# Optimization experiments

Hardware: AMD Instinct MI355X
Metric: run time of the kernel (lower is better)

## Reference

```python
import jax, jax.numpy as jnp
import numpy as np

VOCAB, HIDDEN, EMBED = 100000, 512, 256
N, L = 128, 2048


def setup_inputs() -> dict:
    key = jax.random.key(0)
    k1, k2, k3, k4 = jax.random.split(key, 4)
    X = jax.random.randint(k1, (N, L), 0, VOCAB)
    E = jax.random.normal(k2, (VOCAB, EMBED), dtype=jnp.float32) * 0.02
    # torch Linear: weight (out, in) = (4H, H+E), y = x @ W.T + b
    W_w = jax.random.normal(k3, (4 * HIDDEN, HIDDEN + EMBED), dtype=jnp.float32) * 0.02
    W_b = jax.random.normal(k4, (4 * HIDDEN,), dtype=jnp.float32) * 0.02
    return {"X": X, "E": E, "W_w": W_w, "W_b": W_b}


def reference(X, E, W_w, W_b):
    H = HIDDEN
    Xe = E[X]                      # (N, L, EMBED) embedding lookup
    Xe_t = jnp.transpose(Xe, (1, 0, 2))  # (L, N, EMBED) for scan over time
    n = X.shape[0]
    C0 = jnp.zeros((n, H), dtype=E.dtype)
    H0 = jnp.zeros((n, H), dtype=E.dtype)

    def step(carry, x_t):
        C, Hs = carry
        HcatX = jnp.concatenate([Hs, x_t], axis=1)       # (N, H+E)
        G = HcatX @ W_w.T + W_b                          # (N, 4H)
        F = jax.nn.sigmoid(G[:, :H])
        I = jax.nn.sigmoid(G[:, H:2 * H])
        O = jax.nn.sigmoid(G[:, 2 * H:3 * H])
        Ht = jnp.tanh(G[:, 3 * H:4 * H])
        C_new = F * C + I * Ht
        H_new = O * jnp.tanh(C_new)
        return (C_new, H_new), None

    (C_last, H_last), _ = jax.lax.scan(step, (C0, H0), Xe_t)
    return H_last
```

## Files before the change

kernel.cpp:

```cpp
#include <hip/hip_runtime.h>

#define NB   128
#define LSEQ 2048
#define HID  512
#define EMB  256
#define KD   768
#define NGRP  8
#define NPG   16
#define HBLK  32
#define HPB   16
#define NWG   256
#define NTHR  512
#define RING  4
#define KSL   96
#define FPAD  64
#define SENT 0xFFFFFFFFFFFFFFFFull

#define AT_RLX __ATOMIC_RELAXED
#define SCOPE  __HIP_MEMORY_SCOPE_AGENT

typedef unsigned long long ull;
typedef _Float16 f16;
typedef f16   f16x8 __attribute__((ext_vector_type(8)));
typedef float f32x4 __attribute__((ext_vector_type(4)));

__device__ __forceinline__ float sigf(float x) { return 1.0f / (1.0f + __expf(-x)); }
__device__ __forceinline__ float tanhfast(float x) { return fmaf(-2.0f, 1.0f / (1.0f + __expf(2.0f * x)), 1.0f); }

__device__ __forceinline__ void publish_flag(int* fl, int val, int is_l0) {
    __builtin_amdgcn_s_waitcnt(0);
    if (is_l0) __hip_atomic_store(fl, val, AT_RLX, SCOPE);
}

__global__ void __launch_bounds__(NTHR, 2)
lstm_pers(const int* __restrict__ X, const float* __restrict__ E,
          const float* __restrict__ Ww, const float* __restrict__ Wb,
          float* __restrict__ out, float* __restrict__ ws)
{
    const int tid  = threadIdx.x;
    const int bid  = blockIdx.x;
    const int ng   = bid & (NGRP - 1);
    const int hb   = bid >> 3;
    const int w    = tid >> 6;
    const int lane = tid & 63;
    const int quad = lane >> 4;
    const int m16  = lane & 15;
    const int ks   = w * KSL;
    const int koff = quad * 8;

    __shared__ float red[8][4][16][20];

    f16* Hbuf  = (f16*)ws;
    int* flags = (int*)((char*)ws + (size_t)NGRP * RING * HBLK * NPG * HPB * 2);

    f16x8 wf[4][3];
    #pragma unroll
    for (int g = 0; g < 4; ++g) {
        #pragma unroll
        for (int ti = 0; ti < 3; ++ti) {
            const float* wp = Ww + (size_t)(g * HID + hb * HPB + m16) * KD
                                 + (ks + ti * 32 + koff);
            f16x8 v;
            #pragma unroll
            for (int j = 0; j < 8; ++j) v[j] = (f16)wp[j];
            wf[g][ti] = v;
        }
    }
    f32x4 bias[4], cst = {0, 0, 0, 0};
    if (w == 7) {
        #pragma unroll
        for (int g = 0; g < 4; ++g)
            bias[g] = *(const f32x4*)(Wb + g * HID + hb * HPB + quad * 4);
        #pragma unroll
        for (int s = 2; s <= 3; ++s) {
            ull* z = (ull*)(Hbuf + ((size_t)(ng * RING + s) * HBLK + hb)
                            * (NPG * HPB) + lane * 4);
            __hip_atomic_store(z, SENT, AT_RLX, SCOPE);
        }
    }
    __syncthreads();

    const int* fp6 = flags + (size_t)(ng * HBLK + (lane & (HBLK - 1))) * FPAD;
    int* myflag = &flags[(ng * HBLK + hb) * FPAD];
    const int nh = (ks + 64 < HID) ? 3 : ((ks < HID) ? 1 : 0);

    for (int t = 0; t < LSEQ; ++t) {
        f16x8 bf[3];
        if (ks + 64 >= HID) {
            int xi = X[(ng * NPG + m16) * LSEQ + t];
            const float* eb = E + (size_t)xi * EMB;
            #pragma unroll
            for (int ti = 0; ti < 3; ++ti) {
                int k0 = ks + ti * 32;
                if (k0 >= HID) {
                    const float* ep = eb + (k0 - HID) + koff;
                    f32x4 e0 = *(const f32x4*)(ep);
                    f32x4 e1 = *(const f32x4*)(ep + 4);
                    f16x8 v;
                    #pragma unroll
                    for (int j = 0; j < 4; ++j) { v[j] = (f16)e0[j]; v[4 + j] = (f16)e1[j]; }
                    bf[ti] = v;
                }
            }
        }
        if (w == 6 && t == 1) {
            while (!__all(__hip_atomic_load(fp6, AT_RLX, SCOPE) >= 1))
                __builtin_amdgcn_s_sleep(1);
        }
        __syncthreads();
        if (t == 0) {
            f16x8 z;
            #pragma unroll
            for (int j = 0; j < 8; ++j) z[j] = (f16)0.0f;
            for (int ti = 0; ti < nh; ++ti) bf[ti] = z;
        } else if (nh == 3) {
            const f16* Hc = Hbuf + (size_t)(ng * RING + (t & 3)) * HBLK * (NPG * HPB);
            int ka = ks + koff, kb = ka + 32, kc = kb + 32;
            const ull* h0 = (const ull*)(Hc + (size_t)(ka >> 4) * (NPG * HPB) + m16 * HPB + (ka & 15));
            const ull* h1 = (const ull*)(Hc + (size_t)(kb >> 4) * (NPG * HPB) + m16 * HPB + (kb & 15));
            const ull* h2 = (const ull*)(Hc + (size_t)(kc >> 4) * (NPG * HPB) + m16 * HPB + (kc & 15));
            ull u0, u1, u2, u3, u4, u5;
            for (;;) {
                u0 = __hip_atomic_load(h0,     AT_RLX, SCOPE);
                u1 = __hip_atomic_load(h0 + 1, AT_RLX, SCOPE);
                u2 = __hip_atomic_load(h1,     AT_RLX, SCOPE);
                u3 = __hip_atomic_load(h1 + 1, AT_RLX, SCOPE);
                u4 = __hip_atomic_load(h2,     AT_RLX, SCOPE);
                u5 = __hip_atomic_load(h2 + 1, AT_RLX, SCOPE);
                bool ok = (u0 != SENT) & (u1 != SENT) & (u2 != SENT)
                        & (u3 != SENT) & (u4 != SENT) & (u5 != SENT);
                if (__all(ok)) break;
                __builtin_amdgcn_s_sleep(1);
            }
            union { ull u[2]; f16x8 v; } c;
            c.u[0] = u0; c.u[1] = u1; bf[0] = c.v;
            c.u[0] = u2; c.u[1] = u3; bf[1] = c.v;
            c.u[0] = u4; c.u[1] = u5; bf[2] = c.v;
        } else if (nh == 1) {
            const f16* Hc = Hbuf + (size_t)(ng * RING + (t & 3)) * HBLK * (NPG * HPB);
            int ka = ks + koff;
            const ull* h0 = (const ull*)(Hc + (size_t)(ka >> 4) * (NPG * HPB) + m16 * HPB + (ka & 15));
            ull u0, u1;
            for (;;) {
                u0 = __hip_atomic_load(h0,     AT_RLX, SCOPE);
                u1 = __hip_atomic_load(h0 + 1, AT_RLX, SCOPE);
                if (__all((u0 != SENT) & (u1 != SENT))) break;
                __builtin_amdgcn_s_sleep(1);
            }
            union { ull u[2]; f16x8 v; } c;
            c.u[0] = u0; c.u[1] = u1; bf[0] = c.v;
        }
        f32x4 acc[4] = {{0,0,0,0},{0,0,0,0},{0,0,0,0},{0,0,0,0}};
        #pragma unroll
        for (int ti = 0; ti < 3; ++ti)
            #pragma unroll
            for (int g = 0; g < 4; ++g)
                acc[g] = __builtin_amdgcn_mfma_f32_16x16x32_f16(wf[g][ti], bf[ti], acc[g], 0, 0, 0);

        #pragma unroll
        for (int g = 0; g < 4; ++g)
            *(f32x4*)&red[w][g][m16][quad * 4] = acc[g];
        __syncthreads();

        if (w == 7) {
            f32x4 G[4];
            #pragma unroll
            for (int g = 0; g < 4; ++g) {
                f32x4 s = bias[g];
                #pragma unroll
                for (int wv = 0; wv < 8; ++wv) {
                    f32x4 r = *(const f32x4*)&red[wv][g][m16][quad * 4];
                    s.x += r.x; s.y += r.y; s.z += r.z; s.w += r.w;
                }
                G[g] = s;
            }
            union { f16 h[4]; ull u; } pk;
            f32x4 ov;
            #pragma unroll
            for (int s = 0; s < 4; ++s) {
                float F = sigf(G[0][s]);
                float I = sigf(G[1][s]);
                float O = sigf(G[2][s]);
                float T = tanhfast(G[3][s]);
                cst[s] = fmaf(F, cst[s], I * T);
                float hn = O * tanhfast(cst[s]);
                pk.h[s] = (f16)hn;
                ov[s] = hn;
            }
            if (t < LSEQ - 1) {
                __builtin_amdgcn_s_waitcnt(0);
                f16* Hw = Hbuf + ((size_t)(ng * RING + ((t + 1) & 3)) * HBLK + hb)
                                 * (NPG * HPB);
                __hip_atomic_store((ull*)(Hw + m16 * HPB + quad * 4), pk.u,
                                   AT_RLX, SCOPE);
                if (t == 0) {
                    publish_flag(myflag, 1, lane == 0);
                } else if (t + 3 < LSEQ) {
                    f16* Hs = Hbuf + ((size_t)(ng * RING + ((t + 3) & 3)) * HBLK + hb)
                                     * (NPG * HPB);
                    __hip_atomic_store((ull*)(Hs + m16 * HPB + quad * 4), SENT,
                                       AT_RLX, SCOPE);
                }
            } else {
                *(f32x4*)(out + (size_t)(ng * NPG + m16) * HID + hb * HPB + quad * 4) = ov;
            }
        }
    }
}

extern "C" void kernel_launch(void* const* d_in, const int* in_sizes, int n_in,
                              void* d_out, int out_size, void* d_ws, size_t ws_size,
                              hipStream_t stream) {
    const int*   X   = (const int*)d_in[0];
    const float* E   = (const float*)d_in[1];
    const float* Ww  = (const float*)d_in[2];
    const float* Wb  = (const float*)d_in[3];
    float*       out = (float*)d_out;
    float*       ws  = (float*)d_ws;
    void* args[] = { (void*)&X, (void*)&E, (void*)&Ww, (void*)&Wb,
                     (void*)&out, (void*)&ws };
    hipError_t e = hipLaunchCooperativeKernel((const void*)lstm_pers, dim3(NWG), dim3(NTHR),
                                              args, 0, stream);
    if (e != hipSuccess) {
        hipLaunchKernelGGL(lstm_pers, dim3(NWG), dim3(NTHR), 0, stream,
                           X, E, Ww, Wb, out, ws);
    }
}
```

Before: 6.952 ms.

## Prefetch embeddings into double-buffered LDS and drop one barrier per step

```diff
diff --git a/kernel.cpp b/kernel.cpp
--- a/kernel.cpp
+++ b/kernel.cpp
@@ -16,6 +16,12 @@
 #define FPAD  64
 #define SENT 0xFFFFFFFFFFFFFFFFull
 
+#define RED_FLOATS 10240
+#define RED_BYTES  (RED_FLOATS * 4)
+#define STG_BASE   (2 * RED_BYTES)
+#define STG_BYTES  8192
+#define DSMEM      (STG_BASE + 2 * STG_BYTES)
+
 #define AT_RLX __ATOMIC_RELAXED
 #define SCOPE  __HIP_MEMORY_SCOPE_AGENT
 
@@ -26,6 +32,10 @@
 
 __device__ __forceinline__ float sigf(float x) { return 1.0f / (1.0f + __expf(-x)); }
 __device__ __forceinline__ float tanhfast(float x) { return fmaf(-2.0f, 1.0f / (1.0f + __expf(2.0f * x)), 1.0f); }
+
+__device__ __forceinline__ int stg_off(int buf, int n, int c2) {
+    return STG_BASE + buf * STG_BYTES + n * 512 + (c2 ^ ((n & 7) << 4));
+}
 
 __device__ __forceinline__ void publish_flag(int* fl, int val, int is_l0) {
     __builtin_amdgcn_s_waitcnt(0);
@@ -37,6 +47,8 @@
           const float* __restrict__ Ww, const float* __restrict__ Wb,
           float* __restrict__ out, float* __restrict__ ws)
 {
+    extern __shared__ char dlds[];
+
     const int tid  = threadIdx.x;
     const int bid  = blockIdx.x;
     const int ng   = bid & (NGRP - 1);
@@ -48,8 +60,6 @@
     const int ks   = w * KSL;
     const int koff = quad * 8;
 
-    __shared__ float red[8][4][16][20];
-
     f16* Hbuf  = (f16*)ws;
     int* flags = (int*)((char*)ws + (size_t)NGRP * RING * HBLK * NPG * HPB * 2);
 
@@ -78,6 +88,25 @@
             __hip_atomic_store(z, SENT, AT_RLX, SCOPE);
         }
     }
+
+    const int xrow = (ng * NPG + m16) * LSEQ;
+    const int kcA  = w * 8 + quad;
+    int xN = 0;
+    if (w < 4) {
+        int x0 = X[xrow + 0];
+        xN = X[xrow + 1];
+        const float* ebp = E + (size_t)x0 * EMB;
+        #pragma unroll
+        for (int p = 0; p < 2; ++p) {
+            int kc = kcA + 4 * p;
+            f32x4 e0 = *(const f32x4*)(ebp + kc * 8);
+            f32x4 e1 = *(const f32x4*)(ebp + kc * 8 + 4);
+            f16x8 v;
+            #pragma unroll
+            for (int j = 0; j < 4; ++j) { v[j] = (f16)e0[j]; v[4 + j] = (f16)e1[j]; }
+            *(f16x8*)(dlds + stg_off(0, m16, kc * 16)) = v;
+        }
+    }
     __syncthreads();
 
     const int* fp6 = flags + (size_t)(ng * HBLK + (lane & (HBLK - 1))) * FPAD;
@@ -85,21 +114,28 @@
     const int nh = (ks + 64 < HID) ? 3 : ((ks < HID) ? 1 : 0);
 
     for (int t = 0; t < LSEQ; ++t) {
+        f32x4 ea0, ea1, eb0, eb1; int xF = 0;
+        const bool stg_go = (w < 4) && (t + 1 < LSEQ);
+        if (stg_go) {
+            const float* ebp = E + (size_t)xN * EMB;
+            ea0 = *(const f32x4*)(ebp + kcA * 8);
+            ea1 = *(const f32x4*)(ebp + kcA * 8 + 4);
+            eb0 = *(const f32x4*)(ebp + (kcA + 4) * 8);
+            eb1 = *(const f32x4*)(ebp + (kcA + 4) * 8 + 4);
+        }
+        if (w < 4) {
+            int nidx = (t + 2 < LSEQ) ? t + 2 : LSEQ - 1;
+            xF = X[xrow + nidx];
+        }
+
         f16x8 bf[3];
         if (ks + 64 >= HID) {
-            int xi = X[(ng * NPG + m16) * LSEQ + t];
-            const float* eb = E + (size_t)xi * EMB;
             #pragma unroll
             for (int ti = 0; ti < 3; ++ti) {
                 int k0 = ks + ti * 32;
                 if (k0 >= HID) {
-                    const float* ep = eb + (k0 - HID) + koff;
-                    f32x4 e0 = *(const f32x4*)(ep);
-                    f32x4 e1 = *(const f32x4*)(ep + 4);
-                    f16x8 v;
-                    #pragma unroll
-                    for (int j = 0; j < 4; ++j) { v[j] = (f16)e0[j]; v[4 + j] = (f16)e1[j]; }
-                    bf[ti] = v;
+                    int c2 = (k0 - HID + koff) * 2;
+                    bf[ti] = *(const f16x8*)(dlds + stg_off(t & 1, m16, c2));
                 }
             }
         }
@@ -107,7 +143,8 @@
             while (!__all(__hip_atomic_load(fp6, AT_RLX, SCOPE) >= 1))
                 __builtin_amdgcn_s_sleep(1);
         }
-        __syncthreads();
+        if (t == 1) __syncthreads();
+
         if (t == 0) {
             f16x8 z;
             #pragma unroll
@@ -157,9 +194,22 @@
             for (int g = 0; g < 4; ++g)
                 acc[g] = __builtin_amdgcn_mfma_f32_16x16x32_f16(wf[g][ti], bf[ti], acc[g], 0, 0, 0);
 
+        float* redp = (float*)dlds + (size_t)(t & 1) * RED_FLOATS;
         #pragma unroll
         for (int g = 0; g < 4; ++g)
-            *(f32x4*)&red[w][g][m16][quad * 4] = acc[g];
+            *(f32x4*)&redp[(((w * 4 + g) * 16 + m16) * 20) + quad * 4] = acc[g];
+
+        if (stg_go) {
+            f16x8 va, vb;
+            #pragma unroll
+            for (int j = 0; j < 4; ++j) {
+                va[j] = (f16)ea0[j]; va[4 + j] = (f16)ea1[j];
+                vb[j] = (f16)eb0[j]; vb[4 + j] = (f16)eb1[j];
+            }
+            *(f16x8*)(dlds + stg_off((t + 1) & 1, m16, kcA * 16))       = va;
+            *(f16x8*)(dlds + stg_off((t + 1) & 1, m16, (kcA + 4) * 16)) = vb;
+        }
+        if (w < 4) xN = xF;
         __syncthreads();
 
         if (w == 7) {
@@ -169,7 +219,7 @@
                 f32x4 s = bias[g];
                 #pragma unroll
                 for (int wv = 0; wv < 8; ++wv) {
-                    f32x4 r = *(const f32x4*)&red[wv][g][m16][quad * 4];
+                    f32x4 r = *(const f32x4*)&redp[(((wv * 4 + g) * 16 + m16) * 20) + quad * 4];
                     s.x += r.x; s.y += r.y; s.z += r.z; s.w += r.w;
                 }
                 G[g] = s;
@@ -203,6 +253,7 @@
                 }
             } else {
                 *(f32x4*)(out + (size_t)(ng * NPG + m16) * HID + hb * HPB + quad * 4) = ov;
+                if (lane == 0) __hip_atomic_store(myflag, 0, AT_RLX, SCOPE);
             }
         }
     }
@@ -217,12 +268,21 @@
     const float* Wb  = (const float*)d_in[3];
     float*       out = (float*)d_out;
     float*       ws  = (float*)d_ws;
+
+    static int attr_done = 0;
+    if (!attr_done) {
+        (void)hipFuncSetAttribute((const void*)lstm_pers,
+                                  hipFuncAttributeMaxDynamicSharedMemorySize,
+                                  DSMEM);
+        attr_done = 1;
+    }
+
     void* args[] = { (void*)&X, (void*)&E, (void*)&Ww, (void*)&Wb,
                      (void*)&out, (void*)&ws };
     hipError_t e = hipLaunchCooperativeKernel((const void*)lstm_pers, dim3(NWG), dim3(NTHR),
-                                              args, 0, stream);
+                                              args, DSMEM, stream);
     if (e != hipSuccess) {
-        hipLaunchKernelGGL(lstm_pers, dim3(NWG), dim3(NTHR), 0, stream,
+        hipLaunchKernelGGL(lstm_pers, dim3(NWG), dim3(NTHR), DSMEM, stream,
                            X, E, Ww, Wb, out, ws);
     }
 }
```

New measurement: 7.691 ms. 10.6% more time.

## Split gate epilogue across two waves and double-buffer reduction to drop barrier

Applied to the files above, without the earlier changes.

```diff
diff --git a/kernel.cpp b/kernel.cpp
--- a/kernel.cpp
+++ b/kernel.cpp
@@ -14,18 +14,27 @@
 #define RING  4
 #define KSL   96
 #define FPAD  64
-#define SENT 0xFFFFFFFFFFFFFFFFull
+#define SENT   0xFFFFFFFFFFFFFFFFull
+#define SENT4  0xFFFFFFFFu
+
+#define RED_FLOATS 10240
+#define DSMEM      (2 * RED_FLOATS * 4)
 
 #define AT_RLX __ATOMIC_RELAXED
 #define SCOPE  __HIP_MEMORY_SCOPE_AGENT
 
 typedef unsigned long long ull;
+typedef unsigned int uint;
 typedef _Float16 f16;
 typedef f16   f16x8 __attribute__((ext_vector_type(8)));
 typedef float f32x4 __attribute__((ext_vector_type(4)));
 
 __device__ __forceinline__ float sigf(float x) { return 1.0f / (1.0f + __expf(-x)); }
 __device__ __forceinline__ float tanhfast(float x) { return fmaf(-2.0f, 1.0f / (1.0f + __expf(2.0f * x)), 1.0f); }
+
+__device__ __forceinline__ bool ok8(ull u) {
+    return ((uint)u != SENT4) && ((uint)(u >> 32) != SENT4);
+}
 
 __device__ __forceinline__ void publish_flag(int* fl, int val, int is_l0) {
     __builtin_amdgcn_s_waitcnt(0);
@@ -37,6 +46,8 @@
           const float* __restrict__ Ww, const float* __restrict__ Wb,
           float* __restrict__ out, float* __restrict__ ws)
 {
+    extern __shared__ char dlds[];
+
     const int tid  = threadIdx.x;
     const int bid  = blockIdx.x;
     const int ng   = bid & (NGRP - 1);
@@ -48,8 +59,6 @@
     const int ks   = w * KSL;
     const int koff = quad * 8;
 
-    __shared__ float red[8][4][16][20];
-
     f16* Hbuf  = (f16*)ws;
     int* flags = (int*)((char*)ws + (size_t)NGRP * RING * HBLK * NPG * HPB * 2);
 
@@ -66,16 +75,22 @@
             wf[g][ti] = v;
         }
     }
-    f32x4 bias[4], cst = {0, 0, 0, 0};
-    if (w == 7) {
-        #pragma unroll
-        for (int g = 0; g < 4; ++g)
-            bias[g] = *(const f32x4*)(Wb + g * HID + hb * HPB + quad * 4);
+
+    const int half = w - 6;
+    const int hoff = half * 8 + quad * 2;
+    float2 bias2[4];
+    float  cst0 = 0.0f, cst1 = 0.0f;
+    if (w >= 6) {
+        #pragma unroll
+        for (int g = 0; g < 4; ++g) {
+            const float* bp = Wb + g * HID + hb * HPB + hoff;
+            bias2[g] = make_float2(bp[0], bp[1]);
+        }
         #pragma unroll
         for (int s = 2; s <= 3; ++s) {
-            ull* z = (ull*)(Hbuf + ((size_t)(ng * RING + s) * HBLK + hb)
-                            * (NPG * HPB) + lane * 4);
-            __hip_atomic_store(z, SENT, AT_RLX, SCOPE);
+            uint* z = (uint*)(Hbuf + ((size_t)(ng * RING + s) * HBLK + hb)
+                              * (NPG * HPB) + m16 * HPB + hoff);
+            __hip_atomic_store(z, SENT4, AT_RLX, SCOPE);
         }
     }
     __syncthreads();
@@ -104,10 +119,15 @@
             }
         }
         if (w == 6 && t == 1) {
-            while (!__all(__hip_atomic_load(fp6, AT_RLX, SCOPE) >= 1))
+            for (;;) {
+                int f0 = __hip_atomic_load(fp6,     AT_RLX, SCOPE);
+                int f1 = __hip_atomic_load(fp6 + 8, AT_RLX, SCOPE);
+                if (__all((f0 >= 1) && (f1 >= 1))) break;
                 __builtin_amdgcn_s_sleep(1);
-        }
-        __syncthreads();
+            }
+        }
+        if (t == 1) __syncthreads();
+
         if (t == 0) {
             f16x8 z;
             #pragma unroll
@@ -127,8 +147,8 @@
                 u3 = __hip_atomic_load(h1 + 1, AT_RLX, SCOPE);
                 u4 = __hip_atomic_load(h2,     AT_RLX, SCOPE);
                 u5 = __hip_atomic_load(h2 + 1, AT_RLX, SCOPE);
-                bool ok = (u0 != SENT) & (u1 != SENT) & (u2 != SENT)
-                        & (u3 != SENT) & (u4 != SENT) & (u5 != SENT);
+                bool ok = ok8(u0) & ok8(u1) & ok8(u2)
+                        & ok8(u3) & ok8(u4) & ok8(u5);
                 if (__all(ok)) break;
                 __builtin_amdgcn_s_sleep(1);
             }
@@ -144,7 +164,7 @@
             for (;;) {
                 u0 = __hip_atomic_load(h0,     AT_RLX, SCOPE);
                 u1 = __hip_atomic_load(h0 + 1, AT_RLX, SCOPE);
-                if (__all((u0 != SENT) & (u1 != SENT))) break;
+                if (__all(ok8(u0) & ok8(u1))) break;
                 __builtin_amdgcn_s_sleep(1);
             }
             union { ull u[2]; f16x8 v; } c;
@@ -157,52 +177,54 @@
             for (int g = 0; g < 4; ++g)
                 acc[g] = __builtin_amdgcn_mfma_f32_16x16x32_f16(wf[g][ti], bf[ti], acc[g], 0, 0, 0);
 
+        float* redp = (float*)dlds + (size_t)(t & 1) * RED_FLOATS;
         #pragma unroll
         for (int g = 0; g < 4; ++g)
-            *(f32x4*)&red[w][g][m16][quad * 4] = acc[g];
+            *(f32x4*)&redp[(((w * 4 + g) * 16 + m16) * 20) + quad * 4] = acc[g];
         __syncthreads();
 
-        if (w == 7) {
-            f32x4 G[4];
+        if (w >= 6) {
+            float2 G[4];
             #pragma unroll
             for (int g = 0; g < 4; ++g) {
-                f32x4 s = bias[g];
+                float2 s = bias2[g];
                 #pragma unroll
                 for (int wv = 0; wv < 8; ++wv) {
-                    f32x4 r = *(const f32x4*)&red[wv][g][m16][quad * 4];
-                    s.x += r.x; s.y += r.y; s.z += r.z; s.w += r.w;
+                    const float* r = &redp[(((wv * 4 + g) * 16 + m16) * 20) + hoff];
+                    s.x += r[0]; s.y += r[1];
                 }
                 G[g] = s;
             }
-            union { f16 h[4]; ull u; } pk;
-            f32x4 ov;
-            #pragma unroll
-            for (int s = 0; s < 4; ++s) {
-                float F = sigf(G[0][s]);
-                float I = sigf(G[1][s]);
-                float O = sigf(G[2][s]);
-                float T = tanhfast(G[3][s]);
-                cst[s] = fmaf(F, cst[s], I * T);
-                float hn = O * tanhfast(cst[s]);
-                pk.h[s] = (f16)hn;
-                ov[s] = hn;
-            }
+            float F0 = sigf(G[0].x), F1 = sigf(G[0].y);
+            float I0 = sigf(G[1].x), I1 = sigf(G[1].y);
+            float O0 = sigf(G[2].x), O1 = sigf(G[2].y);
+            float T0 = tanhfast(G[3].x), T1 = tanhfast(G[3].y);
+            cst0 = fmaf(F0, cst0, I0 * T0);
+            cst1 = fmaf(F1, cst1, I1 * T1);
+            float hn0 = O0 * tanhfast(cst0);
+            float hn1 = O1 * tanhfast(cst1);
+            union { f16 h[2]; uint u; } pk;
+            pk.h[0] = (f16)hn0; pk.h[1] = (f16)hn1;
+
             if (t < LSEQ - 1) {
                 __builtin_amdgcn_s_waitcnt(0);
                 f16* Hw = Hbuf + ((size_t)(ng * RING + ((t + 1) & 3)) * HBLK + hb)
                                  * (NPG * HPB);
-                __hip_atomic_store((ull*)(Hw + m16 * HPB + quad * 4), pk.u,
+                __hip_atomic_store((uint*)(Hw + m16 * HPB + hoff), pk.u,
                                    AT_RLX, SCOPE);
                 if (t == 0) {
-                    publish_flag(myflag, 1, lane == 0);
+                    publish_flag(myflag + half * 8, 1, lane == 0);
                 } else if (t + 3 < LSEQ) {
                     f16* Hs = Hbuf + ((size_t)(ng * RING + ((t + 3) & 3)) * HBLK + hb)
                                      * (NPG * HPB);
-                    __hip_atomic_store((ull*)(Hs + m16 * HPB + quad * 4), SENT,
+                    __hip_atomic_store((uint*)(Hs + m16 * HPB + hoff), SENT4,
                                        AT_RLX, SCOPE);
                 }
             } else {
-                *(f32x4*)(out + (size_t)(ng * NPG + m16) * HID + hb * HPB + quad * 4) = ov;
+                float* op = out + (size_t)(ng * NPG + m16) * HID + hb * HPB + hoff;
+                op[0] = hn0; op[1] = hn1;
+                if (lane == 0)
+                    __hip_atomic_store(myflag + half * 8, 0, AT_RLX, SCOPE);
             }
         }
     }
@@ -217,12 +239,21 @@
     const float* Wb  = (const float*)d_in[3];
     float*       out = (float*)d_out;
     float*       ws  = (float*)d_ws;
+
+    static int attr_done = 0;
+    if (!attr_done) {
+        (void)hipFuncSetAttribute((const void*)lstm_pers,
+                                  hipFuncAttributeMaxDynamicSharedMemorySize,
+                                  DSMEM);
+        attr_done = 1;
+    }
+
     void* args[] = { (void*)&X, (void*)&E, (void*)&Ww, (void*)&Wb,
                      (void*)&out, (void*)&ws };
     hipError_t e = hipLaunchCooperativeKernel((const void*)lstm_pers, dim3(NWG), dim3(NTHR),
-                                              args, 0, stream);
+                                              args, DSMEM, stream);
     if (e != hipSuccess) {
-        hipLaunchKernelGGL(lstm_pers, dim3(NWG), dim3(NTHR), 0, stream,
+        hipLaunchKernelGGL(lstm_pers, dim3(NWG), dim3(NTHR), DSMEM, stream,
                            X, E, Ww, Wb, out, ws);
     }
 }
```

New measurement: 6.787 ms. 1.02x faster.
